# Kernel optimization log

Hardware: AMD Instinct MI355X
Metric: run time of the kernel (lower is better)

## Reference

```python
import jax, jax.numpy as jnp
from jax import lax
import numpy as np

MAXLEN, B, D = 2048, 64, 256
CONV_CH = 512

def setup_inputs() -> dict:
    key = jax.random.key(0)
    ks = jax.random.split(key, 10)
    inp = {
        "ctx_val": jax.random.normal(ks[0], (MAXLEN, B, D), jnp.float32),
        "ctx_key": jax.random.normal(ks[1], (MAXLEN, B, D), jnp.float32),
        "ctx_mask": jnp.ones((MAXLEN, B), jnp.float32),
        "attention_past": jax.random.uniform(ks[2], (B, 1, MAXLEN), jnp.float32),
        "ht_query": jax.random.normal(ks[3], (B, D), jnp.float32),
        # learned parameters (torch default inits approximated with scaled normals)
        "W_conv": jax.random.normal(ks[4], (CONV_CH, 1, 3), jnp.float32) * (1.0 / np.sqrt(3.0)),
        "W_query": jax.random.normal(ks[5], (D, D), jnp.float32) * (1.0 / np.sqrt(D)),
        "W_att_past": jax.random.normal(ks[6], (D, CONV_CH), jnp.float32) * (1.0 / np.sqrt(CONV_CH)),
        "b_att_past": jax.random.normal(ks[7], (D,), jnp.float32) * 0.01,
        "W_attn": jax.random.normal(ks[8], (1, D), jnp.float32) * (1.0 / np.sqrt(D)),
        "b_attn": jax.random.normal(ks[9], (1,), jnp.float32) * 0.01,
    }
    return inp

def reference(ctx_val, ctx_key, ctx_mask, attention_past, ht_query,
              W_conv, W_query, W_att_past, b_att_past, W_attn, b_attn):
    # fc_query: (b, D)
    hq = ht_query @ W_query.T
    # conv1d(1->512, k=3, pad=1, no bias): (b, 512, L)
    ap = lax.conv_general_dilated(attention_past, W_conv, window_strides=(1,),
                                  padding=[(1, 1)],
                                  dimension_numbers=("NCH", "OIH", "NCH"))
    # permute(2,0,1) -> (L, b, 512), then fc_att_past -> (L, b, D)
    ap = jnp.einsum("blc,dc->lbd", jnp.transpose(ap, (2, 0, 1)).transpose(1, 0, 2), W_att_past) + b_att_past
    # additive attention score: (L, b)
    s = jnp.tanh(ctx_key + hq[None, :, :] + ap)
    score = jnp.einsum("lbd,d->lb", s, W_attn[0]) + b_attn[0]
    # hard threshold mask, normalize over seq dim
    hard = (score >= 0).astype(jnp.float32) * ctx_mask
    hard = hard / (hard.sum(axis=0) + 1e-10)
    # masked weighted sum over seq dim: (b, D)
    ct = jnp.einsum("lbd,lb->bd", ctx_val, hard)
    return (ct, hard)
```

## Files before the change

### kernel.cpp

```cpp
#include <hip/hip_runtime.h>
#include <math.h>

#define L_MAX 2048
#define BATCH 64
#define DIM   256
#define CCH   512

#define HQ_OFF   0
#define WF_OFF   16384
#define SUMS_OFF 17152
#define HARD_OFF 19200
#define PART_OFF 150272
#define SUMS_STRIDE 32

__device__ __forceinline__ float fast_tanh(float x) {
    float ax = fabsf(x);
    float e  = __expf(2.0f * ax);
    float r  = 1.0f - 2.0f * __builtin_amdgcn_rcpf(e + 1.0f);
    return copysignf(r, x);
}

__global__ __launch_bounds__(256) void prep_kernel(
    const float* __restrict__ ht_query, const float* __restrict__ W_query,
    const float* __restrict__ W_conv,   const float* __restrict__ W_att_past,
    float* __restrict__ hq, float* __restrict__ wf) {
    int t   = threadIdx.x;
    int blk = blockIdx.x;
    __shared__ float q[DIM];
    if (blk < BATCH) {
        q[t] = ht_query[blk * DIM + t];
        __syncthreads();
        const float4* wrow = (const float4*)(W_query + t * DIM);
        float acc = 0.f;
        #pragma unroll 8
        for (int k = 0; k < DIM / 4; k++) {
            float4 wv = wrow[k];
            acc += q[4*k] * wv.x + q[4*k+1] * wv.y + q[4*k+2] * wv.z + q[4*k+3] * wv.w;
        }
        hq[blk * DIM + t] = acc;
    } else {
        int j = blk - BATCH;
        const float4* wrow = (const float4*)(W_att_past + t * CCH);
        float acc = 0.f;
        #pragma unroll 8
        for (int c = 0; c < CCH / 4; c++) {
            float4 wv = wrow[c];
            acc += W_conv[(4*c  ) * 3 + j] * wv.x + W_conv[(4*c+1) * 3 + j] * wv.y
                 + W_conv[(4*c+2) * 3 + j] * wv.z + W_conv[(4*c+3) * 3 + j] * wv.w;
        }
        wf[j * DIM + t] = acc;
    }
}

__global__ __launch_bounds__(256) void score_kernel(
    const float* __restrict__ ctx_key, const float* __restrict__ ctx_mask,
    const float* __restrict__ att_past,
    const float* __restrict__ hq, const float* __restrict__ wf,
    const float* __restrict__ b_att_past, const float* __restrict__ W_attn,
    const float* __restrict__ b_attn,
    float* __restrict__ hard_raw, float* __restrict__ sums) {
    int b     = blockIdx.x & 63;
    int chunk = blockIdx.x >> 6;
    int w     = threadIdx.x >> 6;
    int lane  = threadIdx.x & 63;
    int d0    = lane << 2;
    int l0    = chunk * 64 + w * 16;

    float4 hq4 = *(const float4*)(hq + b * DIM + d0);
    float4 bp  = *(const float4*)(b_att_past + d0);
    hq4.x += bp.x; hq4.y += bp.y; hq4.z += bp.z; hq4.w += bp.w;
    float4 w0  = *(const float4*)(wf + d0);
    float4 w1  = *(const float4*)(wf + DIM + d0);
    float4 w2  = *(const float4*)(wf + 2 * DIM + d0);
    float4 wa  = *(const float4*)(W_attn + d0);
    float battn = b_attn[0];
    const float* apb = att_past + b * L_MAX;

    float cnt = 0.f;
    for (int i = 0; i < 16; i += 4) {
        float4 k4[4];
        float am[4], a0[4], a1[4];
        #pragma unroll
        for (int j = 0; j < 4; j++) {
            int l = l0 + i + j;
            k4[j] = *(const float4*)(ctx_key + (size_t)(l * BATCH + b) * DIM + d0);
            am[j] = (l > 0)         ? apb[l - 1] : 0.f;
            a0[j] = apb[l];
            a1[j] = (l < L_MAX - 1) ? apb[l + 1] : 0.f;
        }
        float p[4];
        #pragma unroll
        for (int j = 0; j < 4; j++) {
            float x0 = k4[j].x + hq4.x + am[j] * w0.x + a0[j] * w1.x + a1[j] * w2.x;
            float x1 = k4[j].y + hq4.y + am[j] * w0.y + a0[j] * w1.y + a1[j] * w2.y;
            float x2 = k4[j].z + hq4.z + am[j] * w0.z + a0[j] * w1.z + a1[j] * w2.z;
            float x3 = k4[j].w + hq4.w + am[j] * w0.w + a0[j] * w1.w + a1[j] * w2.w;
            p[j] = fast_tanh(x0) * wa.x + fast_tanh(x1) * wa.y +
                   fast_tanh(x2) * wa.z + fast_tanh(x3) * wa.w;
        }
        #pragma unroll
        for (int off = 32; off > 0; off >>= 1) {
            p[0] += __shfl_xor(p[0], off, 64);
            p[1] += __shfl_xor(p[1], off, 64);
            p[2] += __shfl_xor(p[2], off, 64);
            p[3] += __shfl_xor(p[3], off, 64);
        }
        if (lane == 0) {
            #pragma unroll
            for (int j = 0; j < 4; j++) {
                int l = l0 + i + j;
                float h = (p[j] + battn >= 0.f) ? ctx_mask[l * BATCH + b] : 0.f;
                hard_raw[l * BATCH + b] = h;
                cnt += h;
            }
        }
    }
    __shared__ float c4[4];
    if (lane == 0) c4[w] = cnt;
    __syncthreads();
    if (threadIdx.x == 0)
        atomicAdd(&sums[b * SUMS_STRIDE], c4[0] + c4[1] + c4[2] + c4[3]);
}

__global__ __launch_bounds__(256) void ct_part_kernel(
    const float* __restrict__ ctx_val, const float* __restrict__ hard_raw,
    float* __restrict__ part) {
    int b     = blockIdx.x & 63;
    int chunk = blockIdx.x >> 6;
    int w     = threadIdx.x >> 6;
    int lane  = threadIdx.x & 63;
    int d0    = lane << 2;
    int l0    = chunk * 64 + w * 16;

    float h[16];
    #pragma unroll
    for (int i = 0; i < 16; i++) h[i] = hard_raw[(l0 + i) * BATCH + b];

    float4 acc = make_float4(0.f, 0.f, 0.f, 0.f);
    #pragma unroll 4
    for (int i = 0; i < 16; i++) {
        if (h[i] != 0.f) {
            int l = l0 + i;
            float4 v = *(const float4*)(ctx_val + (size_t)(l * BATCH + b) * DIM + d0);
            acc.x += v.x * h[i]; acc.y += v.y * h[i];
            acc.z += v.z * h[i]; acc.w += v.w * h[i];
        }
    }
    __shared__ float red[4 * DIM];
    *(float4*)(red + w * DIM + d0) = acc;
    __syncthreads();
    int d = threadIdx.x;
    float s = red[d] + red[DIM + d] + red[2 * DIM + d] + red[3 * DIM + d];
    part[(size_t)(chunk * BATCH + b) * DIM + d] = s;
}

__global__ __launch_bounds__(256) void ct_reduce_kernel(
    const float* __restrict__ part, const float* __restrict__ sums,
    float* __restrict__ ct) {
    int b = blockIdx.x;
    int d = threadIdx.x;
    float s = 0.f;
    #pragma unroll 8
    for (int c = 0; c < 32; c++)
        s += part[(size_t)(c * BATCH + b) * DIM + d];
    float invZ = 1.0f / (sums[b * SUMS_STRIDE] + 1e-10f);
    ct[b * DIM + d] = s * invZ;
}

__global__ __launch_bounds__(256) void norm_kernel(
    const float* __restrict__ hard_raw, const float* __restrict__ sums,
    float* __restrict__ out_hard) {
    int i = blockIdx.x * blockDim.x + threadIdx.x;
    float4 h = *(const float4*)(hard_raw + (size_t)i * 4);
    int b0 = (i * 4) & 63;
    float4 o;
    o.x = h.x / (sums[(b0 + 0) * SUMS_STRIDE] + 1e-10f);
    o.y = h.y / (sums[(b0 + 1) * SUMS_STRIDE] + 1e-10f);
    o.z = h.z / (sums[(b0 + 2) * SUMS_STRIDE] + 1e-10f);
    o.w = h.w / (sums[(b0 + 3) * SUMS_STRIDE] + 1e-10f);
    *(float4*)(out_hard + (size_t)i * 4) = o;
}

extern "C" void kernel_launch(void* const* d_in, const int* in_sizes, int n_in,
                              void* d_out, int out_size, void* d_ws, size_t ws_size,
                              hipStream_t stream) {
    const float* ctx_val    = (const float*)d_in[0];
    const float* ctx_key    = (const float*)d_in[1];
    const float* ctx_mask   = (const float*)d_in[2];
    const float* att_past   = (const float*)d_in[3];
    const float* ht_query   = (const float*)d_in[4];
    const float* W_conv     = (const float*)d_in[5];
    const float* W_query    = (const float*)d_in[6];
    const float* W_att_past = (const float*)d_in[7];
    const float* b_att_past = (const float*)d_in[8];
    const float* W_attn     = (const float*)d_in[9];
    const float* b_attn     = (const float*)d_in[10];

    float* ws   = (float*)d_ws;
    float* hq   = ws + HQ_OFF;
    float* wf   = ws + WF_OFF;
    float* sums = ws + SUMS_OFF;
    float* hard = ws + HARD_OFF;
    float* part = ws + PART_OFF;

    float* out_ct   = (float*)d_out;
    float* out_hard = (float*)d_out + BATCH * DIM;

    hipMemsetAsync(sums, 0, BATCH * SUMS_STRIDE * sizeof(float), stream);

    prep_kernel<<<BATCH + 3, 256, 0, stream>>>(ht_query, W_query, W_conv, W_att_past, hq, wf);

    score_kernel<<<BATCH * 32, 256, 0, stream>>>(
        ctx_key, ctx_mask, att_past, hq, wf, b_att_past, W_attn, b_attn, hard, sums);

    ct_part_kernel<<<BATCH * 32, 256, 0, stream>>>(ctx_val, hard, part);

    ct_reduce_kernel<<<BATCH, 256, 0, stream>>>(part, sums, out_ct);

    norm_kernel<<<(L_MAX * BATCH) / (4 * 256), 256, 0, stream>>>(hard, sums, out_hard);
}
```

Before: 336.5 us.

## Fuse score and weighted-sum kernels, merge tail kernels, drop memset

Folds the ctx_val weighted accumulation into the score kernel, so each block reads ctx_val for the rows it has just scored without a separate pass or re-reading hard_raw. The final reduction and hard normalisation become one launch, and the sums buffer is zeroed inside prep_kernel instead of by a hipMemsetAsync. This cuts launch count and intermediate traffic. The ctx_val loads now wait on the score reduction inside the same loop, which may add latency per row.

```diff
diff --git a/kernel.cpp b/kernel.cpp
--- a/kernel.cpp
+++ b/kernel.cpp
@@ -23,9 +23,10 @@
 __global__ __launch_bounds__(256) void prep_kernel(
     const float* __restrict__ ht_query, const float* __restrict__ W_query,
     const float* __restrict__ W_conv,   const float* __restrict__ W_att_past,
-    float* __restrict__ hq, float* __restrict__ wf) {
+    float* __restrict__ hq, float* __restrict__ wf, float* __restrict__ sums) {
     int t   = threadIdx.x;
     int blk = blockIdx.x;
+    if (blk == 0 && t < BATCH) sums[t * SUMS_STRIDE] = 0.f;
     __shared__ float q[DIM];
     if (blk < BATCH) {
         q[t] = ht_query[blk * DIM + t];
@@ -52,13 +53,14 @@
     }
 }
 
-__global__ __launch_bounds__(256) void score_kernel(
-    const float* __restrict__ ctx_key, const float* __restrict__ ctx_mask,
-    const float* __restrict__ att_past,
+__global__ __launch_bounds__(256) void fused_kernel(
+    const float* __restrict__ ctx_key, const float* __restrict__ ctx_val,
+    const float* __restrict__ ctx_mask, const float* __restrict__ att_past,
     const float* __restrict__ hq, const float* __restrict__ wf,
     const float* __restrict__ b_att_past, const float* __restrict__ W_attn,
     const float* __restrict__ b_attn,
-    float* __restrict__ hard_raw, float* __restrict__ sums) {
+    float* __restrict__ hard_raw, float* __restrict__ sums,
+    float* __restrict__ part) {
     int b     = blockIdx.x & 63;
     int chunk = blockIdx.x >> 6;
     int w     = threadIdx.x >> 6;
@@ -77,6 +79,8 @@
     const float* apb = att_past + b * L_MAX;
 
     float cnt = 0.f;
+    float4 acc = make_float4(0.f, 0.f, 0.f, 0.f);
+
     for (int i = 0; i < 16; i += 4) {
         float4 k4[4];
         float am[4], a0[4], a1[4];
@@ -105,80 +109,56 @@
             p[2] += __shfl_xor(p[2], off, 64);
             p[3] += __shfl_xor(p[3], off, 64);
         }
-        if (lane == 0) {
-            #pragma unroll
-            for (int j = 0; j < 4; j++) {
-                int l = l0 + i + j;
-                float h = (p[j] + battn >= 0.f) ? ctx_mask[l * BATCH + b] : 0.f;
-                hard_raw[l * BATCH + b] = h;
-                cnt += h;
+        #pragma unroll
+        for (int j = 0; j < 4; j++) {
+            int l = l0 + i + j;
+            float h = (p[j] + battn >= 0.f) ? ctx_mask[l * BATCH + b] : 0.f;
+            if (lane == 0) hard_raw[l * BATCH + b] = h;
+            cnt += h;
+            if (h != 0.f) {
+                float4 v = *(const float4*)(ctx_val + (size_t)(l * BATCH + b) * DIM + d0);
+                acc.x += v.x * h; acc.y += v.y * h;
+                acc.z += v.z * h; acc.w += v.w * h;
             }
         }
     }
+
+    __shared__ float red[4 * DIM];
+    *(float4*)(red + w * DIM + d0) = acc;
     __shared__ float c4[4];
     if (lane == 0) c4[w] = cnt;
     __syncthreads();
+    int d = threadIdx.x;
+    float s = red[d] + red[DIM + d] + red[2 * DIM + d] + red[3 * DIM + d];
+    part[(size_t)(chunk * BATCH + b) * DIM + d] = s;
     if (threadIdx.x == 0)
         atomicAdd(&sums[b * SUMS_STRIDE], c4[0] + c4[1] + c4[2] + c4[3]);
 }
 
-__global__ __launch_bounds__(256) void ct_part_kernel(
-    const float* __restrict__ ctx_val, const float* __restrict__ hard_raw,
-    float* __restrict__ part) {
-    int b     = blockIdx.x & 63;
-    int chunk = blockIdx.x >> 6;
-    int w     = threadIdx.x >> 6;
-    int lane  = threadIdx.x & 63;
-    int d0    = lane << 2;
-    int l0    = chunk * 64 + w * 16;
-
-    float h[16];
-    #pragma unroll
-    for (int i = 0; i < 16; i++) h[i] = hard_raw[(l0 + i) * BATCH + b];
-
-    float4 acc = make_float4(0.f, 0.f, 0.f, 0.f);
-    #pragma unroll 4
-    for (int i = 0; i < 16; i++) {
-        if (h[i] != 0.f) {
-            int l = l0 + i;
-            float4 v = *(const float4*)(ctx_val + (size_t)(l * BATCH + b) * DIM + d0);
-            acc.x += v.x * h[i]; acc.y += v.y * h[i];
-            acc.z += v.z * h[i]; acc.w += v.w * h[i];
-        }
+__global__ __launch_bounds__(256) void tail_kernel(
+    const float* __restrict__ part, const float* __restrict__ hard_raw,
+    const float* __restrict__ sums,
+    float* __restrict__ ct, float* __restrict__ out_hard) {
+    if (blockIdx.x < BATCH) {
+        int b = blockIdx.x;
+        int d = threadIdx.x;
+        float s = 0.f;
+        #pragma unroll 8
+        for (int c = 0; c < 32; c++)
+            s += part[(size_t)(c * BATCH + b) * DIM + d];
+        float invZ = 1.0f / (sums[b * SUMS_STRIDE] + 1e-10f);
+        ct[b * DIM + d] = s * invZ;
+    } else {
+        int i = (blockIdx.x - BATCH) * 256 + threadIdx.x;
+        float4 h = *(const float4*)(hard_raw + (size_t)i * 4);
+        int b0 = (i * 4) & 63;
+        float4 o;
+        o.x = h.x / (sums[(b0 + 0) * SUMS_STRIDE] + 1e-10f);
+        o.y = h.y / (sums[(b0 + 1) * SUMS_STRIDE] + 1e-10f);
+        o.z = h.z / (sums[(b0 + 2) * SUMS_STRIDE] + 1e-10f);
+        o.w = h.w / (sums[(b0 + 3) * SUMS_STRIDE] + 1e-10f);
+        *(float4*)(out_hard + (size_t)i * 4) = o;
     }
-    __shared__ float red[4 * DIM];
-    *(float4*)(red + w * DIM + d0) = acc;
-    __syncthreads();
-    int d = threadIdx.x;
-    float s = red[d] + red[DIM + d] + red[2 * DIM + d] + red[3 * DIM + d];
-    part[(size_t)(chunk * BATCH + b) * DIM + d] = s;
-}
-
-__global__ __launch_bounds__(256) void ct_reduce_kernel(
-    const float* __restrict__ part, const float* __restrict__ sums,
-    float* __restrict__ ct) {
-    int b = blockIdx.x;
-    int d = threadIdx.x;
-    float s = 0.f;
-    #pragma unroll 8
-    for (int c = 0; c < 32; c++)
-        s += part[(size_t)(c * BATCH + b) * DIM + d];
-    float invZ = 1.0f / (sums[b * SUMS_STRIDE] + 1e-10f);
-    ct[b * DIM + d] = s * invZ;
-}
-
-__global__ __launch_bounds__(256) void norm_kernel(
-    const float* __restrict__ hard_raw, const float* __restrict__ sums,
-    float* __restrict__ out_hard) {
-    int i = blockIdx.x * blockDim.x + threadIdx.x;
-    float4 h = *(const float4*)(hard_raw + (size_t)i * 4);
-    int b0 = (i * 4) & 63;
-    float4 o;
-    o.x = h.x / (sums[(b0 + 0) * SUMS_STRIDE] + 1e-10f);
-    o.y = h.y / (sums[(b0 + 1) * SUMS_STRIDE] + 1e-10f);
-    o.z = h.z / (sums[(b0 + 2) * SUMS_STRIDE] + 1e-10f);
-    o.w = h.w / (sums[(b0 + 3) * SUMS_STRIDE] + 1e-10f);
-    *(float4*)(out_hard + (size_t)i * 4) = o;
 }
 
 extern "C" void kernel_launch(void* const* d_in, const int* in_sizes, int n_in,
@@ -206,16 +186,12 @@
     float* out_ct   = (float*)d_out;
     float* out_hard = (float*)d_out + BATCH * DIM;
 
-    hipMemsetAsync(sums, 0, BATCH * SUMS_STRIDE * sizeof(float), stream);
+    prep_kernel<<<BATCH + 3, 256, 0, stream>>>(
+        ht_query, W_query, W_conv, W_att_past, hq, wf, sums);
 
-    prep_kernel<<<BATCH + 3, 256, 0, stream>>>(ht_query, W_query, W_conv, W_att_past, hq, wf);
+    fused_kernel<<<BATCH * 32, 256, 0, stream>>>(
+        ctx_key, ctx_val, ctx_mask, att_past, hq, wf, b_att_past, W_attn, b_attn,
+        hard, sums, part);
 
-    score_kernel<<<BATCH * 32, 256, 0, stream>>>(
-        ctx_key, ctx_mask, att_past, hq, wf, b_att_past, W_attn, b_attn, hard, sums);
-
-    ct_part_kernel<<<BATCH * 32, 256, 0, stream>>>(ctx_val, hard, part);
-
-    ct_reduce_kernel<<<BATCH, 256, 0, stream>>>(part, sums, out_ct);
-
-    norm_kernel<<<(L_MAX * BATCH) / (4 * 256), 256, 0, stream>>>(hard, sums, out_hard);
+    tail_kernel<<<BATCH + 128, 256, 0, stream>>>(part, hard, sums, out_ct, out_hard);
 }
```

After: 337.8 us. Within noise of the previous version (+0.4%).
